# Kernel optimization log

Measured on AMD Instinct MI355X. Metric: run time of the kernel, lower is better.

## Reference

```python
import jax, jax.numpy as jnp
import numpy as np

N_NODES = 100000
N_EDGES = 800000
EDGE_NAMES = ["ei_connected_to", "ei_ordered_next", "ei_represents", "ei_represented_by",
              "ei_neighboring_vertical", "ei_neighboring_horizontal", "ei_contains",
              "ei_order", "ei_perpendicular"]
AGGRS_L2 = ["sum", "sum", "mean", "mean", "sum", "sum", "mean"]


def _glorot(key, shape):
    fan_in, fan_out = shape[-2], shape[-1]
    s = (2.0 / (fan_in + fan_out)) ** 0.5
    return jax.random.normal(key, shape, dtype=jnp.float32) * s


def setup_inputs() -> dict:
    key = jax.random.key(0)
    ks = iter(jax.random.split(key, 32))
    inp = {"x": jax.random.normal(next(ks), (N_NODES, 6), dtype=jnp.float32)}
    for name in EDGE_NAMES:
        inp[name] = jax.random.randint(next(ks), (2, N_EDGES), 0, N_NODES, dtype=jnp.int32)
    inp.update(
        W0n=_glorot(next(ks), (2, 6, 16)), W0r=_glorot(next(ks), (2, 6, 16)),
        b0=jnp.zeros((2, 16), jnp.float32),
        W1n=_glorot(next(ks), (2, 16, 32)), W1r=_glorot(next(ks), (2, 16, 32)),
        b1=jnp.zeros((2, 32), jnp.float32),
        P1=_glorot(next(ks), (16, 32)), pb1=jnp.zeros((32,), jnp.float32),
        W2n=_glorot(next(ks), (7, 32, 64)), W2r=_glorot(next(ks), (7, 32, 64)),
        b2=jnp.zeros((7, 64), jnp.float32),
        P2=_glorot(next(ks), (32, 64)), pb2=jnp.zeros((64,), jnp.float32),
    )
    return inp


def _hetero_conv(x, edges, aggrs, Wn, Wr, b):
    # Per-relation GraphConv: out_d = aggr(x[src]->dst) @ Wn_r + x @ Wr_r + b_r,
    # summed across relations (HeteroConv aggr='sum'). Loop is over a small fixed
    # set of relation types (structurally distinct), not data dims.
    n = x.shape[0]
    out = jnp.zeros((n, Wn.shape[-1]), x.dtype)
    for i, (ei, aggr) in enumerate(zip(edges, aggrs)):
        src, dst = ei[0], ei[1]
        msg = jax.ops.segment_sum(x[src], dst, num_segments=n)  # scatter-add gather
        if aggr == "mean":
            cnt = jax.ops.segment_sum(jnp.ones_like(dst, dtype=x.dtype), dst, num_segments=n)
            msg = msg / jnp.maximum(cnt, 1.0)[:, None]
        out = out + msg @ Wn[i] + x @ Wr[i] + b[i]
    return out


def reference(x, W0n, W0r, b0, W1n, W1r, b1, P1, pb1, W2n, W2r, b2, P2, pb2,
              ei_connected_to, ei_ordered_next, ei_represents, ei_represented_by,
              ei_neighboring_vertical, ei_neighboring_horizontal, ei_contains,
              ei_order, ei_perpendicular):
    e01 = [ei_connected_to, ei_ordered_next]
    e2 = [ei_represents, ei_represented_by, ei_neighboring_vertical,
          ei_neighboring_horizontal, ei_contains, ei_order, ei_perpendicular]
    # local head: 6 -> 16 (two sum relations)
    h = _hetero_conv(x, e01, ["sum", "sum"], W0n, W0r, b0)
    # residual block 1: 16 -> 32 (same two sum relations, linear residual projection)
    h = jax.nn.relu(_hetero_conv(h, e01, ["sum", "sum"], W1n, W1r, b1) + h @ P1 + pb1)
    # residual block 2: 32 -> 64 (seven relations, sum/mean aggregation)
    h = jax.nn.relu(_hetero_conv(h, e2, AGGRS_L2, W2n, W2r, b2) + h @ P2 + pb2)
    # final elementwise relu from SemanticModule.forward
    return jax.nn.relu(h)
```

## Files before the change

kernel.cpp:

```cpp
#include <hip/hip_runtime.h>

#define NN 100000
#define NE 800000
#define NRG 128
#define SPAN 784
#define CAP 8192
#define NBIN (9 * NRG)

typedef _Float16 f16;
typedef __attribute__((ext_vector_type(4))) _Float16 f16x4;
typedef __attribute__((ext_vector_type(8))) _Float16 f16x8;
typedef __attribute__((ext_vector_type(4))) float f32x4;
typedef __attribute__((ext_vector_type(2))) float f32x2;

struct EPtrs { const int* s[9]; const int* d[9]; };

__global__ __launch_bounds__(256) void prep_weights(
    const float* __restrict__ W0n, const float* __restrict__ W0r, const float* __restrict__ b0,
    const float* __restrict__ W1n, const float* __restrict__ W1r, const float* __restrict__ b1,
    const float* __restrict__ P1,  const float* __restrict__ pb1,
    const float* __restrict__ W2n, const float* __restrict__ W2r, const float* __restrict__ b2,
    const float* __restrict__ P2,  const float* __restrict__ pb2,
    float* __restrict__ wc0, float* __restrict__ bc0,
    float* __restrict__ wc1, float* __restrict__ bc1,
    f16*   __restrict__ b2frag, float* __restrict__ bc2,
    int*   __restrict__ cursor)
{
    int tid = threadIdx.x;
    for (int t = tid; t < NBIN; t += 256) cursor[t] = 0;

    for (int t = tid; t < 18 * 16; t += 256) {
        int row = t >> 4, col = t & 15;
        float v;
        if (row < 6)       v = W0n[row * 16 + col];
        else if (row < 12) v = W0n[96 + (row - 6) * 16 + col];
        else               v = W0r[(row - 12) * 16 + col] + W0r[96 + (row - 12) * 16 + col];
        wc0[t] = v;
    }
    for (int t = tid; t < 16; t += 256) bc0[t] = b0[t] + b0[16 + t];

    for (int t = tid; t < 48 * 32; t += 256) {
        int row = t >> 5, col = t & 31;
        float v;
        if (row < 16)      v = W1n[row * 32 + col];
        else if (row < 32) v = W1n[512 + (row - 16) * 32 + col];
        else { int rr = row - 32; v = W1r[rr * 32 + col] + W1r[512 + rr * 32 + col] + P1[rr * 32 + col]; }
        wc1[t] = v;
    }
    for (int t = tid; t < 32; t += 256) bc1[t] = b1[t] + b1[32 + t] + pb1[t];

    for (int t = tid; t < 256 * 64; t += 256) {
        int j = t & 7, lane = (t >> 3) & 63, ntk = t >> 9;
        int nt = ntk & 3, kt = ntk >> 2;
        int k = kt * 32 + (lane >> 4) * 8 + j;
        int n = nt * 16 + (lane & 15);
        float v;
        if (k < 224) v = W2n[k * 64 + n];
        else {
            int rr = k - 224;
            v = P2[rr * 64 + n];
            #pragma unroll
            for (int r = 0; r < 7; ++r) v += W2r[r * 2048 + rr * 64 + n];
        }
        b2frag[t] = (f16)v;
    }
    for (int t = tid; t < 64; t += 256) {
        float v = pb2[t];
        #pragma unroll
        for (int r = 0; r < 7; ++r) v += b2[r * 64 + t];
        bc2[t] = v;
    }
}

__global__ __launch_bounds__(256) void passA(EPtrs ep, int* __restrict__ cursor,
                                             unsigned* __restrict__ binbuf)
{
    int r = blockIdx.y;
    int e0 = blockIdx.x * 4096;
    int cnt = min(4096, NE - e0);
    int tid = threadIdx.x;
    __shared__ int h[NRG];
    __shared__ int bs[NRG + 1];
    __shared__ int cl[NRG];
    __shared__ int gb[NRG];
    __shared__ int auxtot;
    __shared__ unsigned pk[4096];

    if (tid < NRG) h[tid] = 0;
    __syncthreads();

    const int* dp = ep.d[r];
    const int* sp = ep.s[r];
    unsigned wv[16];
    int rgk[16];
    #pragma unroll
    for (int k = 0; k < 16; ++k) {
        int e = e0 + k * 256 + tid;
        rgk[k] = -1;
        if (e < NE) {
            int d = dp[e];
            int sv = sp[e];
            int g = d / SPAN;
            int l = d - g * SPAN;
            wv[k] = ((unsigned)l << 17) | (unsigned)sv;
            rgk[k] = g;
            atomicAdd(&h[g], 1);
        }
    }
    __syncthreads();

    int vcnt = 0, incl = 0;
    if (tid < NRG) {
        vcnt = h[tid];
        incl = vcnt;
        int lane = tid & 63;
        #pragma unroll
        for (int ofs = 1; ofs < 64; ofs <<= 1) {
            int u = __shfl_up(incl, ofs, 64);
            if (lane >= ofs) incl += u;
        }
        if (tid == 63) auxtot = incl;
    }
    __syncthreads();
    if (tid < NRG) {
        int excl = incl - vcnt + ((tid >= 64) ? auxtot : 0);
        bs[tid] = excl;
        cl[tid] = excl;
        gb[tid] = (vcnt > 0) ? atomicAdd(&cursor[r * NRG + tid], vcnt) : 0;
        if (tid == NRG - 1) bs[NRG] = excl + vcnt;
    }
    __syncthreads();

    #pragma unroll
    for (int k = 0; k < 16; ++k) {
        if (rgk[k] >= 0) {
            int p = atomicAdd(&cl[rgk[k]], 1);
            pk[p] = wv[k];
        }
    }
    __syncthreads();

    for (int i = tid; i < cnt; i += 256) {
        int loB = 0, hiB = NRG;
        while (hiB - loB > 1) {
            int mid = (loB + hiB) >> 1;
            if (bs[mid] <= i) loB = mid; else hiB = mid;
        }
        int b = loB;
        int pos = gb[b] + (i - bs[b]);
        if (pos < CAP)
            binbuf[((size_t)(r * NRG + b)) * CAP + pos] = pk[i];
    }
}

__global__ __launch_bounds__(256) void passB(const unsigned* __restrict__ binbuf,
                                             const int* __restrict__ cursor,
                                             int* __restrict__ deg, int* __restrict__ off,
                                             int* __restrict__ eidx)
{
    int bin = blockIdx.x;
    int r = bin >> 7, rg = bin & (NRG - 1);
    int lo = rg * SPAN;
    int n_here = min(SPAN, NN - lo);
    int tid = threadIdx.x;
    __shared__ int h[SPAN];
    __shared__ int wsum[4];
    __shared__ int stage[CAP];

    int sz = min(cursor[bin], CAP);
    const unsigned* bp = binbuf + (size_t)bin * CAP;

    for (int i = tid; i < SPAN; i += 256) h[i] = 0;
    __syncthreads();

    unsigned wv[32];
    int rk[32];
    #pragma unroll
    for (int k = 0; k < 32; ++k) {
        int e = tid + k * 256;
        if (e < sz) {
            unsigned w = bp[e];
            wv[k] = w;
            rk[k] = atomicAdd(&h[w >> 17], 1);
        }
    }
    __syncthreads();

    int i0 = tid * 4;
    int dstash[4];
    int s = 0;
    #pragma unroll
    for (int k = 0; k < 4; ++k) {
        int i = i0 + k;
        int v = (i < SPAN) ? h[i] : 0;
        dstash[k] = v;
        s += v;
    }
    int lane = tid & 63, wid = tid >> 6;
    int incl = s;
    #pragma unroll
    for (int ofs = 1; ofs < 64; ofs <<= 1) {
        int u = __shfl_up(incl, ofs, 64);
        if (lane >= ofs) incl += u;
    }
    if (lane == 63) wsum[wid] = incl;
    __syncthreads();
    if (tid == 0) {
        int a = wsum[0], b = wsum[1], c = wsum[2];
        wsum[0] = 0; wsum[1] = a; wsum[2] = a + b; wsum[3] = a + b + c;
    }
    __syncthreads();
    int run = incl - s + wsum[wid];
    int base = bin * CAP;
    #pragma unroll
    for (int k = 0; k < 4; ++k) {
        int i = i0 + k;
        if (i < SPAN) {
            int v = dstash[k];
            h[i] = run;
            if (i < n_here) {
                deg[r * NN + lo + i] = v;
                off[r * NN + lo + i] = base + run + v;
            }
            run += v;
        }
    }
    __syncthreads();

    #pragma unroll
    for (int k = 0; k < 32; ++k) {
        int e = tid + k * 256;
        if (e < sz) {
            unsigned w = wv[k];
            stage[h[w >> 17] + rk[k]] = (int)(w & 0x1FFFF);
        }
    }
    __syncthreads();
    for (int i = tid; i < sz; i += 256) eidx[base + i] = stage[i];
}

__global__ __launch_bounds__(256) void t0f(const float* __restrict__ x,
                                           const int* __restrict__ deg, const int* __restrict__ off,
                                           const int* __restrict__ eidx,
                                           const float* __restrict__ wc0, const float* __restrict__ bc0,
                                           f16* __restrict__ h0h)
{
    __shared__ float sw[288 + 16];
    for (int t = threadIdx.x; t < 304; t += 256) sw[t] = (t < 288) ? wc0[t] : bc0[t - 288];
    __syncthreads();
    int t = blockIdx.x * 256 + threadIdx.x;
    int node = t >> 2;
    if (node >= NN) return;
    int l = t & 3;
    int r = l >> 1, p = l & 1;

    float m[6] = {0, 0, 0, 0, 0, 0};
    {
        int e1 = off[r * NN + node];
        int e0 = e1 - deg[r * NN + node];
        int e = e0 + p;
        for (; e + 2 < e1; e += 4) {
            int sA = eidx[e], sB = eidx[e + 2];
            const float2* pA = reinterpret_cast<const float2*>(x + (size_t)sA * 6);
            const float2* pB = reinterpret_cast<const float2*>(x + (size_t)sB * 6);
            float2 a0 = pA[0], a1 = pA[1], a2 = pA[2];
            float2 b0 = pB[0], b1 = pB[1], b2 = pB[2];
            m[0] += a0.x + b0.x; m[1] += a0.y + b0.y;
            m[2] += a1.x + b1.x; m[3] += a1.y + b1.y;
            m[4] += a2.x + b2.x; m[5] += a2.y + b2.y;
        }
        if (e < e1) {
            int sA = eidx[e];
            const float2* pA = reinterpret_cast<const float2*>(x + (size_t)sA * 6);
            float2 a0 = pA[0], a1 = pA[1], a2 = pA[2];
            m[0] += a0.x; m[1] += a0.y; m[2] += a1.x; m[3] += a1.y; m[4] += a2.x; m[5] += a2.y;
        }
    }
    float mo[6];
    #pragma unroll
    for (int k = 0; k < 6; ++k) {
        m[k] += __shfl_xor(m[k], 1, 64);
        mo[k] = __shfl_xor(m[k], 2, 64);
    }
    int baseOwn = r * 96, baseOth = (1 - r) * 96;
    float xv[6];
    {
        const float2* xp = reinterpret_cast<const float2*>(x + (size_t)node * 6);
        float2 a = xp[0], b = xp[1], c = xp[2];
        xv[0] = a.x; xv[1] = a.y; xv[2] = b.x; xv[3] = b.y; xv[4] = c.x; xv[5] = c.y;
    }
    int dc = l * 4;
    float acc[4];
    #pragma unroll
    for (int j = 0; j < 4; ++j) acc[j] = sw[288 + dc + j];
    #pragma unroll
    for (int k = 0; k < 6; ++k) {
        #pragma unroll
        for (int j = 0; j < 4; ++j) {
            acc[j] = fmaf(m[k],  sw[baseOwn + k * 16 + dc + j], acc[j]);
            acc[j] = fmaf(mo[k], sw[baseOth + k * 16 + dc + j], acc[j]);
            acc[j] = fmaf(xv[k], sw[192 + k * 16 + dc + j], acc[j]);
        }
    }
    f16x4 o;
    #pragma unroll
    for (int j = 0; j < 4; ++j) o[j] = (f16)acc[j];
    *reinterpret_cast<f16x4*>(h0h + (size_t)node * 16 + dc) = o;
}

__global__ __launch_bounds__(256) void g1t(const int* __restrict__ deg, const int* __restrict__ off,
                                           const int* __restrict__ eidx, const f16* __restrict__ h0h,
                                           const float* __restrict__ wc1, const float* __restrict__ bc1,
                                           f16* __restrict__ h1h, unsigned* __restrict__ h1q)
{
    __shared__ float sw[1536 + 32];
    __shared__ float ms[64][33];
    for (int t = threadIdx.x; t < 1568; t += 256) sw[t] = (t < 1536) ? wc1[t] : bc1[t - 1536];

    int tid = threadIdx.x;
    int nloc = tid >> 2, l = tid & 3;
    int node = blockIdx.x * 64 + nloc;

    if (node < NN) {
        #pragma unroll 1
        for (int r = 0; r < 2; ++r) {
            int e1 = off[r * NN + node];
            int e0 = e1 - deg[r * NN + node];
            float a0 = 0.f, a1 = 0.f, a2 = 0.f, a3 = 0.f;
            int e = e0;
            for (; e + 4 <= e1; e += 4) {
                int sA = eidx[e], sB = eidx[e + 1], sC = eidx[e + 2], sD = eidx[e + 3];
                f16x4 vA = *reinterpret_cast<const f16x4*>(h0h + (size_t)sA * 16 + l * 4);
                f16x4 vB = *reinterpret_cast<const f16x4*>(h0h + (size_t)sB * 16 + l * 4);
                f16x4 vC = *reinterpret_cast<const f16x4*>(h0h + (size_t)sC * 16 + l * 4);
                f16x4 vD = *reinterpret_cast<const f16x4*>(h0h + (size_t)sD * 16 + l * 4);
                a0 += (float)vA[0] + (float)vB[0] + (float)vC[0] + (float)vD[0];
                a1 += (float)vA[1] + (float)vB[1] + (float)vC[1] + (float)vD[1];
                a2 += (float)vA[2] + (float)vB[2] + (float)vC[2] + (float)vD[2];
                a3 += (float)vA[3] + (float)vB[3] + (float)vC[3] + (float)vD[3];
            }
            for (; e < e1; ++e) {
                f16x4 v = *reinterpret_cast<const f16x4*>(h0h + (size_t)eidx[e] * 16 + l * 4);
                a0 += (float)v[0]; a1 += (float)v[1]; a2 += (float)v[2]; a3 += (float)v[3];
            }
            ms[nloc][r * 16 + l * 4 + 0] = a0;
            ms[nloc][r * 16 + l * 4 + 1] = a1;
            ms[nloc][r * 16 + l * 4 + 2] = a2;
            ms[nloc][r * 16 + l * 4 + 3] = a3;
        }
    }
    __syncthreads();
    if (node >= NN) return;

    int c0 = l * 8;
    float acc[8];
    #pragma unroll
    for (int j = 0; j < 8; ++j) acc[j] = sw[1536 + c0 + j];
    #pragma unroll
    for (int k = 0; k < 32; ++k) {
        float s = ms[nloc][k];
        #pragma unroll
        for (int j = 0; j < 8; ++j) acc[j] = fmaf(s, sw[k * 32 + c0 + j], acc[j]);
    }
    {
        const f16x8* hp = reinterpret_cast<const f16x8*>(h0h + (size_t)node * 16);
        f16x8 a = hp[0], b = hp[1];
        #pragma unroll
        for (int k = 0; k < 8; ++k) {
            float s0 = (float)a[k], s1 = (float)b[k];
            #pragma unroll
            for (int j = 0; j < 8; ++j)
                acc[j] = fmaf(s0, sw[(32 + k) * 32 + c0 + j], fmaf(s1, sw[(40 + k) * 32 + c0 + j], acc[j]));
        }
    }
    #pragma unroll
    for (int j = 0; j < 8; ++j) acc[j] = fmaxf(acc[j], 0.f);

    f16x8 o;
    #pragma unroll
    for (int j = 0; j < 8; ++j) o[j] = (f16)acc[j];
    *reinterpret_cast<f16x8*>(h1h + (size_t)node * 32 + c0) = o;

    int w0 = __builtin_amdgcn_cvt_pk_fp8_f32(acc[0], acc[1], 0, false);
    w0 = __builtin_amdgcn_cvt_pk_fp8_f32(acc[2], acc[3], w0, true);
    int w1 = __builtin_amdgcn_cvt_pk_fp8_f32(acc[4], acc[5], 0, false);
    w1 = __builtin_amdgcn_cvt_pk_fp8_f32(acc[6], acc[7], w1, true);
    *reinterpret_cast<uint2*>(h1q + (size_t)node * 8 + l * 2) = make_uint2((unsigned)w0, (unsigned)w1);
}

__global__ __launch_bounds__(256, 8) void g2t2(const int* __restrict__ deg, const int* __restrict__ off,
                                               const int* __restrict__ eidx, const unsigned* __restrict__ h1q,
                                               const f16* __restrict__ h1h, const f16* __restrict__ b2frag,
                                               const float* __restrict__ bc2, float* __restrict__ out)
{
    __shared__ f16 cat[16][264];

    int tid = threadIdx.x;
    int nloc = tid >> 4;
    int lane16 = tid & 15;
    int node = blockIdx.x * 16 + nloc;

    if (lane16 >= 14) {
        int part = lane16 - 14;
        const f16x8* hp = reinterpret_cast<const f16x8*>(h1h + (size_t)node * 32 + part * 16);
        f16x8 v0 = hp[0], v1 = hp[1];
        *reinterpret_cast<f16x8*>(&cat[nloc][224 + part * 16]) = v0;
        *reinterpret_cast<f16x8*>(&cat[nloc][224 + part * 16 + 8]) = v1;
    } else {
        int r = lane16 >> 1;
        int half = lane16 & 1;
        int d = deg[(r + 2) * NN + node];
        int e1 = off[(r + 2) * NN + node];
        int e0 = e1 - d;

        f32x2 acc[8];
        #pragma unroll
        for (int q = 0; q < 8; ++q) acc[q] = (f32x2){0.f, 0.f};

        const uint4* tbl = reinterpret_cast<const uint4*>(h1q);
        int e = e0;
        for (; e + 2 <= e1; e += 2) {
            int sA = eidx[e], sB = eidx[e + 1];
            uint4 qA = tbl[(size_t)sA * 2 + half];
            uint4 qB = tbl[(size_t)sB * 2 + half];
            acc[0] += __builtin_amdgcn_cvt_pk_f32_fp8(qA.x, false);
            acc[1] += __builtin_amdgcn_cvt_pk_f32_fp8(qA.x, true);
            acc[2] += __builtin_amdgcn_cvt_pk_f32_fp8(qA.y, false);
            acc[3] += __builtin_amdgcn_cvt_pk_f32_fp8(qA.y, true);
            acc[4] += __builtin_amdgcn_cvt_pk_f32_fp8(qA.z, false);
            acc[5] += __builtin_amdgcn_cvt_pk_f32_fp8(qA.z, true);
            acc[6] += __builtin_amdgcn_cvt_pk_f32_fp8(qA.w, false);
            acc[7] += __builtin_amdgcn_cvt_pk_f32_fp8(qA.w, true);
            acc[0] += __builtin_amdgcn_cvt_pk_f32_fp8(qB.x, false);
            acc[1] += __builtin_amdgcn_cvt_pk_f32_fp8(qB.x, true);
            acc[2] += __builtin_amdgcn_cvt_pk_f32_fp8(qB.y, false);
            acc[3] += __builtin_amdgcn_cvt_pk_f32_fp8(qB.y, true);
            acc[4] += __builtin_amdgcn_cvt_pk_f32_fp8(qB.z, false);
            acc[5] += __builtin_amdgcn_cvt_pk_f32_fp8(qB.z, true);
            acc[6] += __builtin_amdgcn_cvt_pk_f32_fp8(qB.w, false);
            acc[7] += __builtin_amdgcn_cvt_pk_f32_fp8(qB.w, true);
        }
        if (e < e1) {
            int sA = eidx[e];
            uint4 qA = tbl[(size_t)sA * 2 + half];
            acc[0] += __builtin_amdgcn_cvt_pk_f32_fp8(qA.x, false);
            acc[1] += __builtin_amdgcn_cvt_pk_f32_fp8(qA.x, true);
            acc[2] += __builtin_amdgcn_cvt_pk_f32_fp8(qA.y, false);
            acc[3] += __builtin_amdgcn_cvt_pk_f32_fp8(qA.y, true);
            acc[4] += __builtin_amdgcn_cvt_pk_f32_fp8(qA.z, false);
            acc[5] += __builtin_amdgcn_cvt_pk_f32_fp8(qA.z, true);
            acc[6] += __builtin_amdgcn_cvt_pk_f32_fp8(qA.w, false);
            acc[7] += __builtin_amdgcn_cvt_pk_f32_fp8(qA.w, true);
        }

        float sc = (r == 2 || r == 3 || r == 6) ? (1.0f / (float)max(d, 1)) : 1.0f;
        f16x8 o0, o1;
        #pragma unroll
        for (int q = 0; q < 4; ++q) {
            o0[q * 2 + 0] = (f16)(acc[q][0] * sc);
            o0[q * 2 + 1] = (f16)(acc[q][1] * sc);
            o1[q * 2 + 0] = (f16)(acc[4 + q][0] * sc);
            o1[q * 2 + 1] = (f16)(acc[4 + q][1] * sc);
        }
        *reinterpret_cast<f16x8*>(&cat[nloc][r * 32 + half * 16]) = o0;
        *reinterpret_cast<f16x8*>(&cat[nloc][r * 32 + half * 16 + 8]) = o1;
    }

    int lane = tid & 63, w = tid >> 6;
    int quad = lane >> 4, col0 = lane & 15;
    float bcv = bc2[w * 16 + col0];

    f16x8 bfr[8];
    #pragma unroll
    for (int kt = 0; kt < 8; ++kt)
        bfr[kt] = *reinterpret_cast<const f16x8*>(b2frag + ((size_t)(kt * 4 + w) * 64 + lane) * 8);

    __syncthreads();

    f32x4 acc = (f32x4){0.f, 0.f, 0.f, 0.f};
    #pragma unroll
    for (int kt = 0; kt < 8; ++kt) {
        f16x8 a = *reinterpret_cast<const f16x8*>(&cat[col0][kt * 32 + quad * 8]);
        acc = __builtin_amdgcn_mfma_f32_16x16x32_f16(a, bfr[kt], acc, 0, 0, 0);
    }

    int row0 = blockIdx.x * 16 + quad * 4;
    #pragma unroll
    for (int i = 0; i < 4; ++i)
        out[(size_t)(row0 + i) * 64 + w * 16 + col0] = fmaxf(acc[i] + bcv, 0.f);
}

extern "C" void kernel_launch(void* const* d_in, const int* in_sizes, int n_in,
                              void* d_out, int out_size, void* d_ws, size_t ws_size,
                              hipStream_t stream)
{
    const float* x = (const float*)d_in[0];
    EPtrs ep;
    for (int i = 0; i < 9; ++i) { const int* p = (const int*)d_in[1 + i]; ep.s[i] = p; ep.d[i] = p + NE; }
    const float* W0n = (const float*)d_in[10]; const float* W0r = (const float*)d_in[11];
    const float* b0  = (const float*)d_in[12];
    const float* W1n = (const float*)d_in[13]; const float* W1r = (const float*)d_in[14];
    const float* b1  = (const float*)d_in[15];
    const float* P1  = (const float*)d_in[16]; const float* pb1 = (const float*)d_in[17];
    const float* W2n = (const float*)d_in[18]; const float* W2r = (const float*)d_in[19];
    const float* b2  = (const float*)d_in[20];
    const float* P2  = (const float*)d_in[21]; const float* pb2 = (const float*)d_in[22];
    float* out = (float*)d_out;
    char* ws = (char*)d_ws;

    size_t off_b = 0;
    auto alloc = [&](size_t b) { size_t o = off_b; off_b += (b + 255) & ~(size_t)255; return o; };
    size_t o_wc0 = alloc(288 * 4);   size_t o_bc0 = alloc(16 * 4);
    size_t o_wc1 = alloc(1536 * 4);  size_t o_bc1 = alloc(32 * 4);
    size_t o_b2f = alloc(16384 * 2); size_t o_bc2 = alloc(64 * 4);
    size_t o_h0h = alloc((size_t)NN * 16 * 2);
    size_t o_h1q = alloc((size_t)NN * 32);
    size_t o_h1h = alloc((size_t)NN * 32 * 2);
    size_t o_bin = alloc((size_t)NBIN * CAP * 4);
    size_t o_deg = alloc((size_t)9 * NN * 4);
    size_t o_off = alloc((size_t)9 * NN * 4);
    size_t o_eid = alloc((size_t)NBIN * CAP * 4);
    size_t o_cur = alloc((size_t)NBIN * 4);
    (void)ws_size;

    float* wc0 = (float*)(ws + o_wc0); float* bc0 = (float*)(ws + o_bc0);
    float* wc1 = (float*)(ws + o_wc1); float* bc1 = (float*)(ws + o_bc1);
    f16*   b2f = (f16*)(ws + o_b2f);   float* bc2 = (float*)(ws + o_bc2);
    f16*   h0h = (f16*)(ws + o_h0h);
    unsigned* h1q = (unsigned*)(ws + o_h1q);
    f16*   h1h = (f16*)(ws + o_h1h);
    unsigned* binbuf = (unsigned*)(ws + o_bin);
    int*   deg = (int*)(ws + o_deg);
    int*   offp = (int*)(ws + o_off);
    int*   eid = (int*)(ws + o_eid);
    int*   cur = (int*)(ws + o_cur);

    dim3 B(256);
    prep_weights<<<1, B, 0, stream>>>(W0n, W0r, b0, W1n, W1r, b1, P1, pb1,
                                      W2n, W2r, b2, P2, pb2,
                                      wc0, bc0, wc1, bc1, b2f, bc2, cur);
    passA<<<dim3((NE + 4095) / 4096, 9), B, 0, stream>>>(ep, cur, binbuf);
    passB<<<NBIN, B, 0, stream>>>(binbuf, cur, deg, offp, eid);

    t0f<<<(NN * 4 + 255) / 256, B, 0, stream>>>(x, deg, offp, eid, wc0, bc0, h0h);
    g1t<<<(NN + 63) / 64, B, 0, stream>>>(deg, offp, eid, h0h, wc1, bc1, h1h, h1q);
    g2t2<<<NN / 16, B, 0, stream>>>(deg, offp, eid, h1q, h1h, b2f, bc2, out);
}
```

Measured before the change: 310.8 us.

## Double bin count, tag binned edges with their bin, and widen g1t per-node threads

The edge binning now uses 256 dst-range bins of half the span and capacity. passA keeps a per-edge bin byte in shared memory, so the scatter step no longer needs a binary search over bin starts. passB processes smaller bins with fewer registers per thread. g1t now gives each node 8 threads, one per relation and column quarter, so the two relation gathers run in parallel and each thread computes 4 outputs instead of 8. The price is more blocks and bins, more cursor atomics, and a smaller per-bin capacity that could overflow on skewed inputs.

```diff
diff --git a/kernel.cpp b/kernel.cpp
--- a/kernel.cpp
+++ b/kernel.cpp
@@ -2,9 +2,9 @@
 
 #define NN 100000
 #define NE 800000
-#define NRG 128
-#define SPAN 784
-#define CAP 8192
+#define NRG 256
+#define SPAN 392
+#define CAP 4096
 #define NBIN (9 * NRG)
 
 typedef _Float16 f16;
@@ -80,13 +80,14 @@
     int cnt = min(4096, NE - e0);
     int tid = threadIdx.x;
     __shared__ int h[NRG];
-    __shared__ int bs[NRG + 1];
+    __shared__ int bs[NRG];
     __shared__ int cl[NRG];
     __shared__ int gb[NRG];
-    __shared__ int auxtot;
+    __shared__ int wsumA[4];
     __shared__ unsigned pk[4096];
-
-    if (tid < NRG) h[tid] = 0;
+    __shared__ unsigned char pkb[4096];
+
+    h[tid] = 0;
     __syncthreads();
 
     const int* dp = ep.d[r];
@@ -109,26 +110,25 @@
     }
     __syncthreads();
 
-    int vcnt = 0, incl = 0;
-    if (tid < NRG) {
-        vcnt = h[tid];
-        incl = vcnt;
-        int lane = tid & 63;
-        #pragma unroll
-        for (int ofs = 1; ofs < 64; ofs <<= 1) {
-            int u = __shfl_up(incl, ofs, 64);
-            if (lane >= ofs) incl += u;
-        }
-        if (tid == 63) auxtot = incl;
-    }
-    __syncthreads();
-    if (tid < NRG) {
-        int excl = incl - vcnt + ((tid >= 64) ? auxtot : 0);
-        bs[tid] = excl;
-        cl[tid] = excl;
-        gb[tid] = (vcnt > 0) ? atomicAdd(&cursor[r * NRG + tid], vcnt) : 0;
-        if (tid == NRG - 1) bs[NRG] = excl + vcnt;
-    }
+    int vcnt = h[tid];
+    int lane = tid & 63, wid = tid >> 6;
+    int incl = vcnt;
+    #pragma unroll
+    for (int ofs = 1; ofs < 64; ofs <<= 1) {
+        int u = __shfl_up(incl, ofs, 64);
+        if (lane >= ofs) incl += u;
+    }
+    if (lane == 63) wsumA[wid] = incl;
+    __syncthreads();
+    if (tid == 0) {
+        int a = wsumA[0], b = wsumA[1], c = wsumA[2];
+        wsumA[0] = 0; wsumA[1] = a; wsumA[2] = a + b; wsumA[3] = a + b + c;
+    }
+    __syncthreads();
+    int excl = incl - vcnt + wsumA[wid];
+    bs[tid] = excl;
+    cl[tid] = excl;
+    gb[tid] = (vcnt > 0) ? atomicAdd(&cursor[r * NRG + tid], vcnt) : 0;
     __syncthreads();
 
     #pragma unroll
@@ -136,20 +136,16 @@
         if (rgk[k] >= 0) {
             int p = atomicAdd(&cl[rgk[k]], 1);
             pk[p] = wv[k];
+            pkb[p] = (unsigned char)rgk[k];
         }
     }
     __syncthreads();
 
     for (int i = tid; i < cnt; i += 256) {
-        int loB = 0, hiB = NRG;
-        while (hiB - loB > 1) {
-            int mid = (loB + hiB) >> 1;
-            if (bs[mid] <= i) loB = mid; else hiB = mid;
-        }
-        int b = loB;
-        int pos = gb[b] + (i - bs[b]);
+        int g = pkb[i];
+        int pos = gb[g] + (i - bs[g]);
         if (pos < CAP)
-            binbuf[((size_t)(r * NRG + b)) * CAP + pos] = pk[i];
+            binbuf[((size_t)(r * NRG + g)) * CAP + pos] = pk[i];
     }
 }
 
@@ -159,7 +155,7 @@
                                              int* __restrict__ eidx)
 {
     int bin = blockIdx.x;
-    int r = bin >> 7, rg = bin & (NRG - 1);
+    int r = bin >> 8, rg = bin & (NRG - 1);
     int lo = rg * SPAN;
     int n_here = min(SPAN, NN - lo);
     int tid = threadIdx.x;
@@ -173,10 +169,10 @@
     for (int i = tid; i < SPAN; i += 256) h[i] = 0;
     __syncthreads();
 
-    unsigned wv[32];
-    int rk[32];
-    #pragma unroll
-    for (int k = 0; k < 32; ++k) {
+    unsigned wv[16];
+    int rk[16];
+    #pragma unroll
+    for (int k = 0; k < 16; ++k) {
         int e = tid + k * 256;
         if (e < sz) {
             unsigned w = bp[e];
@@ -186,11 +182,11 @@
     }
     __syncthreads();
 
-    int i0 = tid * 4;
-    int dstash[4];
+    int i0 = tid * 2;
+    int dstash[2];
     int s = 0;
     #pragma unroll
-    for (int k = 0; k < 4; ++k) {
+    for (int k = 0; k < 2; ++k) {
         int i = i0 + k;
         int v = (i < SPAN) ? h[i] : 0;
         dstash[k] = v;
@@ -213,7 +209,7 @@
     int run = incl - s + wsum[wid];
     int base = bin * CAP;
     #pragma unroll
-    for (int k = 0; k < 4; ++k) {
+    for (int k = 0; k < 2; ++k) {
         int i = i0 + k;
         if (i < SPAN) {
             int v = dstash[k];
@@ -228,7 +224,7 @@
     __syncthreads();
 
     #pragma unroll
-    for (int k = 0; k < 32; ++k) {
+    for (int k = 0; k < 16; ++k) {
         int e = tid + k * 256;
         if (e < sz) {
             unsigned w = wv[k];
@@ -314,53 +310,51 @@
                                            f16* __restrict__ h1h, unsigned* __restrict__ h1q)
 {
     __shared__ float sw[1536 + 32];
-    __shared__ float ms[64][33];
+    __shared__ float ms[32][33];
     for (int t = threadIdx.x; t < 1568; t += 256) sw[t] = (t < 1536) ? wc1[t] : bc1[t - 1536];
 
     int tid = threadIdx.x;
-    int nloc = tid >> 2, l = tid & 3;
-    int node = blockIdx.x * 64 + nloc;
+    int nloc = tid >> 3, l = tid & 7;
+    int r = l >> 2, dq = l & 3;
+    int node = blockIdx.x * 32 + nloc;
 
     if (node < NN) {
-        #pragma unroll 1
-        for (int r = 0; r < 2; ++r) {
-            int e1 = off[r * NN + node];
-            int e0 = e1 - deg[r * NN + node];
-            float a0 = 0.f, a1 = 0.f, a2 = 0.f, a3 = 0.f;
-            int e = e0;
-            for (; e + 4 <= e1; e += 4) {
-                int sA = eidx[e], sB = eidx[e + 1], sC = eidx[e + 2], sD = eidx[e + 3];
-                f16x4 vA = *reinterpret_cast<const f16x4*>(h0h + (size_t)sA * 16 + l * 4);
-                f16x4 vB = *reinterpret_cast<const f16x4*>(h0h + (size_t)sB * 16 + l * 4);
-                f16x4 vC = *reinterpret_cast<const f16x4*>(h0h + (size_t)sC * 16 + l * 4);
-                f16x4 vD = *reinterpret_cast<const f16x4*>(h0h + (size_t)sD * 16 + l * 4);
-                a0 += (float)vA[0] + (float)vB[0] + (float)vC[0] + (float)vD[0];
-                a1 += (float)vA[1] + (float)vB[1] + (float)vC[1] + (float)vD[1];
-                a2 += (float)vA[2] + (float)vB[2] + (float)vC[2] + (float)vD[2];
-                a3 += (float)vA[3] + (float)vB[3] + (float)vC[3] + (float)vD[3];
-            }
-            for (; e < e1; ++e) {
-                f16x4 v = *reinterpret_cast<const f16x4*>(h0h + (size_t)eidx[e] * 16 + l * 4);
-                a0 += (float)v[0]; a1 += (float)v[1]; a2 += (float)v[2]; a3 += (float)v[3];
-            }
-            ms[nloc][r * 16 + l * 4 + 0] = a0;
-            ms[nloc][r * 16 + l * 4 + 1] = a1;
-            ms[nloc][r * 16 + l * 4 + 2] = a2;
-            ms[nloc][r * 16 + l * 4 + 3] = a3;
-        }
+        int e1 = off[r * NN + node];
+        int e0 = e1 - deg[r * NN + node];
+        float a0 = 0.f, a1 = 0.f, a2 = 0.f, a3 = 0.f;
+        int e = e0;
+        for (; e + 4 <= e1; e += 4) {
+            int sA = eidx[e], sB = eidx[e + 1], sC = eidx[e + 2], sD = eidx[e + 3];
+            f16x4 vA = *reinterpret_cast<const f16x4*>(h0h + (size_t)sA * 16 + dq * 4);
+            f16x4 vB = *reinterpret_cast<const f16x4*>(h0h + (size_t)sB * 16 + dq * 4);
+            f16x4 vC = *reinterpret_cast<const f16x4*>(h0h + (size_t)sC * 16 + dq * 4);
+            f16x4 vD = *reinterpret_cast<const f16x4*>(h0h + (size_t)sD * 16 + dq * 4);
+            a0 += (float)vA[0] + (float)vB[0] + (float)vC[0] + (float)vD[0];
+            a1 += (float)vA[1] + (float)vB[1] + (float)vC[1] + (float)vD[1];
+            a2 += (float)vA[2] + (float)vB[2] + (float)vC[2] + (float)vD[2];
+            a3 += (float)vA[3] + (float)vB[3] + (float)vC[3] + (float)vD[3];
+        }
+        for (; e < e1; ++e) {
+            f16x4 v = *reinterpret_cast<const f16x4*>(h0h + (size_t)eidx[e] * 16 + dq * 4);
+            a0 += (float)v[0]; a1 += (float)v[1]; a2 += (float)v[2]; a3 += (float)v[3];
+        }
+        ms[nloc][r * 16 + dq * 4 + 0] = a0;
+        ms[nloc][r * 16 + dq * 4 + 1] = a1;
+        ms[nloc][r * 16 + dq * 4 + 2] = a2;
+        ms[nloc][r * 16 + dq * 4 + 3] = a3;
     }
     __syncthreads();
     if (node >= NN) return;
 
-    int c0 = l * 8;
-    float acc[8];
-    #pragma unroll
-    for (int j = 0; j < 8; ++j) acc[j] = sw[1536 + c0 + j];
+    int c0 = l * 4;
+    float acc[4];
+    #pragma unroll
+    for (int j = 0; j < 4; ++j) acc[j] = sw[1536 + c0 + j];
     #pragma unroll
     for (int k = 0; k < 32; ++k) {
         float s = ms[nloc][k];
         #pragma unroll
-        for (int j = 0; j < 8; ++j) acc[j] = fmaf(s, sw[k * 32 + c0 + j], acc[j]);
+        for (int j = 0; j < 4; ++j) acc[j] = fmaf(s, sw[k * 32 + c0 + j], acc[j]);
     }
     {
         const f16x8* hp = reinterpret_cast<const f16x8*>(h0h + (size_t)node * 16);
@@ -369,23 +363,21 @@
         for (int k = 0; k < 8; ++k) {
             float s0 = (float)a[k], s1 = (float)b[k];
             #pragma unroll
-            for (int j = 0; j < 8; ++j)
+            for (int j = 0; j < 4; ++j)
                 acc[j] = fmaf(s0, sw[(32 + k) * 32 + c0 + j], fmaf(s1, sw[(40 + k) * 32 + c0 + j], acc[j]));
         }
     }
     #pragma unroll
-    for (int j = 0; j < 8; ++j) acc[j] = fmaxf(acc[j], 0.f);
-
-    f16x8 o;
-    #pragma unroll
-    for (int j = 0; j < 8; ++j) o[j] = (f16)acc[j];
-    *reinterpret_cast<f16x8*>(h1h + (size_t)node * 32 + c0) = o;
+    for (int j = 0; j < 4; ++j) acc[j] = fmaxf(acc[j], 0.f);
+
+    f16x4 o;
+    #pragma unroll
+    for (int j = 0; j < 4; ++j) o[j] = (f16)acc[j];
+    *reinterpret_cast<f16x4*>(h1h + (size_t)node * 32 + c0) = o;
 
     int w0 = __builtin_amdgcn_cvt_pk_fp8_f32(acc[0], acc[1], 0, false);
     w0 = __builtin_amdgcn_cvt_pk_fp8_f32(acc[2], acc[3], w0, true);
-    int w1 = __builtin_amdgcn_cvt_pk_fp8_f32(acc[4], acc[5], 0, false);
-    w1 = __builtin_amdgcn_cvt_pk_fp8_f32(acc[6], acc[7], w1, true);
-    *reinterpret_cast<uint2*>(h1q + (size_t)node * 8 + l * 2) = make_uint2((unsigned)w0, (unsigned)w1);
+    h1q[(size_t)node * 8 + l] = (unsigned)w0;
 }
 
 __global__ __launch_bounds__(256, 8) void g2t2(const int* __restrict__ deg, const int* __restrict__ off,
@@ -543,6 +535,6 @@
     passB<<<NBIN, B, 0, stream>>>(binbuf, cur, deg, offp, eid);
 
     t0f<<<(NN * 4 + 255) / 256, B, 0, stream>>>(x, deg, offp, eid, wc0, bc0, h0h);
-    g1t<<<(NN + 63) / 64, B, 0, stream>>>(deg, offp, eid, h0h, wc1, bc1, h1h, h1q);
+    g1t<<<(NN + 31) / 32, B, 0, stream>>>(deg, offp, eid, h0h, wc1, bc1, h1h, h1q);
     g2t2<<<NN / 16, B, 0, stream>>>(deg, offp, eid, h1q, h1h, b2f, bc2, out);
 }
```

Result: no change. 310.2 us (-0.2%).
